# Performance work log

Measured on AMD Instinct MI355X. Metric: run time of the kernel, lower is better.

Reference implementation:

```python
import jax, jax.numpy as jnp
import numpy as np

N_NODES = 50000
N_EDGES = 800000
D_IN = 128
D_HID = 128
D_OUT = 128


def setup_inputs() -> dict:
    key = jax.random.key(0)
    ks = jax.random.split(key, 5)
    x = jax.random.normal(ks[0], (N_NODES, D_IN), dtype=jnp.float32)
    edge_index = jax.random.randint(ks[1], (2, N_EDGES), 0, N_NODES, dtype=jnp.int64)
    # Glorot-ish init for the two GCN linear weights (PyG uses glorot)
    W1 = jax.random.normal(ks[2], (D_IN, D_HID), dtype=jnp.float32) * (1.0 / np.sqrt(D_IN))
    b1 = jnp.zeros((D_HID,), dtype=jnp.float32)
    W2 = jax.random.normal(ks[3], (D_HID, D_OUT), dtype=jnp.float32) * (1.0 / np.sqrt(D_HID))
    b2 = jnp.zeros((D_OUT,), dtype=jnp.float32)
    return {"x": x, "edge_index": edge_index, "W1": W1, "b1": b1, "W2": W2, "b2": b2}


def _gcn_layer(x, W, b, src, dst, dinv):
    """PyG GCNConv: h = xW; out[j] = sum_{(i->j)} dinv[i]*dinv[j]*h[i] + dinv[j]^2*h[j] (self-loop) + b."""
    n = x.shape[0]
    h = x @ W                                   # [N, D_out]
    coef = (dinv[src] * dinv[dst])[:, None]     # [E, 1] symmetric norm
    msg = h[src] * coef                         # [E, D_out] gather + scale
    agg = jax.ops.segment_sum(msg, dst, num_segments=n)  # scatter-add
    agg = agg + h * (dinv * dinv)[:, None]      # self-loop contribution
    return agg + b


def reference(x, edge_index, W1, b1, W2, b2):
    src = edge_index[0]
    dst = edge_index[1]
    n = x.shape[0]
    # degree over target nodes, including the added self-loop (+1)
    deg = jax.ops.segment_sum(jnp.ones_like(dst, dtype=x.dtype), dst, num_segments=n) + 1.0
    dinv = jax.lax.rsqrt(deg)
    h = jax.nn.relu(_gcn_layer(x, W1, b1, src, dst, dinv))
    return _gcn_layer(h, W2, b2, src, dst, dinv)
```

## Files before the change

kernel.cpp:

```cpp
#include <hip/hip_runtime.h>
#include <hip/hip_fp16.h>

#define NN 50000
#define NE 800000
#define D 128
#define NBLK ((NN + 255) / 256)
#define NBLK_GEMM ((NN + 63) / 64)

typedef __attribute__((ext_vector_type(8))) _Float16 f16x8;
typedef __attribute__((ext_vector_type(8))) short short8;
typedef __attribute__((ext_vector_type(4))) float f32x4;

__global__ __launch_bounds__(256) void k_init(int* __restrict__ cnt,
                                              const float* __restrict__ W1, const float* __restrict__ W2,
                                              char* __restrict__ img1, char* __restrict__ img2) {
    int b = blockIdx.x;
    if (b < NBLK) {
        int i = b * 256 + threadIdx.x;
        if (i < NN) cnt[i] = 0;
    } else {
        int pb = b - NBLK;
        const float* W = (pb < 64) ? W1 : W2;
        char* img = (pb < 64) ? img1 : img2;
        int e = (pb & 63) * 256 + threadIdx.x;
        int k = e >> 7, n = e & 127;
        float f = W[e];
        __half hi = __float2half_rn(f);
        float rem = f - __half2float(hi);
        __half lo = __float2half_rn(rem);
        unsigned off = (unsigned)((n << 8) + (k << 1)) ^ (unsigned)((n & 7) << 4);
        *(__half*)(img + off) = hi;
        *(__half*)(img + 32768 + off) = lo;
    }
}

__global__ __launch_bounds__(256) void k_count(const int* __restrict__ dst, int* __restrict__ cnt,
                                               unsigned short* __restrict__ rank) {
    int e = blockIdx.x * 256 + threadIdx.x;
    if (e < NE) rank[e] = (unsigned short)atomicAdd(&cnt[dst[e]], 1);
}

__global__ __launch_bounds__(256) void k_scan_partial(const int* __restrict__ cnt, int* __restrict__ blockSums) {
    __shared__ int s[256];
    int t = threadIdx.x;
    int i = blockIdx.x * 256 + t;
    s[t] = (i < NN) ? cnt[i] : 0;
    __syncthreads();
    for (int off = 128; off > 0; off >>= 1) {
        if (t < off) s[t] += s[t + off];
        __syncthreads();
    }
    if (t == 0) blockSums[blockIdx.x] = s[0];
}

__global__ __launch_bounds__(256) void k_scan_final(const int* __restrict__ cnt, const int* __restrict__ blockSums,
                                                    int* __restrict__ row_ptr, float* __restrict__ dinv) {
    __shared__ int s[256];
    int t = threadIdx.x;

    s[t] = (t < NBLK && t < (int)blockIdx.x) ? blockSums[t] : 0;
    __syncthreads();
    for (int off = 128; off > 0; off >>= 1) {
        if (t < off) s[t] += s[t + off];
        __syncthreads();
    }
    int blockOff = s[0];
    __syncthreads();

    int i = blockIdx.x * 256 + t;
    int v = (i < NN) ? cnt[i] : 0;
    s[t] = v;
    __syncthreads();
    for (int off = 1; off < 256; off <<= 1) {
        int y = (t >= off) ? s[t - off] : 0;
        __syncthreads();
        s[t] += y;
        __syncthreads();
    }
    if (i < NN) {
        row_ptr[i] = s[t] - v + blockOff;
        dinv[i] = rsqrtf((float)v + 1.0f);
    }
    if (blockIdx.x == 0 && t == 0) row_ptr[NN] = NE;
}

template <bool RELU_IN, bool A_FP16>
static __device__ __forceinline__ void gemm_core(char* lds, const void* __restrict__ Av,
                                                 const char* __restrict__ wimg, __half* __restrict__ H,
                                                 int bid, int t) {
    {
        const float4* gv = (const float4*)wimg;
        float4* lv = (float4*)lds;
#pragma unroll
        for (int i = 0; i < 16; ++i) lv[i * 256 + t] = gv[i * 256 + t];
    }
    __syncthreads();

    const int lane = t & 63;
    const int wv = t >> 6;
    const int r0 = bid * 64 + wv * 16;
    const int rl = lane & 15;
    const int g = lane >> 4;
    int arow = r0 + rl;
    if (arow >= NN) arow = NN - 1;

    f32x4 acc[8];
#pragma unroll
    for (int j = 0; j < 8; ++j) acc[j] = (f32x4){0.f, 0.f, 0.f, 0.f};

#pragma unroll
    for (int ks = 0; ks < 4; ++ks) {
        f16x8 a;
        if (A_FP16) {
            const __half* A = (const __half*)Av;
            float4 raw = *(const float4*)(A + (size_t)arow * D + ks * 32 + g * 8);
            if (RELU_IN) {
                short8 s = __builtin_bit_cast(short8, raw);
#pragma unroll
                for (int i = 0; i < 8; ++i) s[i] = (s[i] & (short)0x8000) ? (short)0 : s[i];
                a = __builtin_bit_cast(f16x8, s);
            } else {
                a = __builtin_bit_cast(f16x8, raw);
            }
        } else {
            const float* A = (const float*)Av;
            const float* ar = A + (size_t)arow * D + ks * 32 + g * 8;
            float4 p0 = *(const float4*)ar;
            float4 p1 = *(const float4*)(ar + 4);
            float av8[8] = {p0.x, p0.y, p0.z, p0.w, p1.x, p1.y, p1.z, p1.w};
#pragma unroll
            for (int i = 0; i < 8; ++i) {
                float f = RELU_IN ? fmaxf(av8[i], 0.f) : av8[i];
                a[i] = (_Float16)f;
            }
        }
        const int kofs = (ks * 32 + g * 8) << 1;
#pragma unroll
        for (int j = 0; j < 8; ++j) {
            int n = j * 16 + rl;
            unsigned off = (unsigned)((n << 8) + kofs) ^ (unsigned)((n & 7) << 4);
            f16x8 bh = *(const f16x8*)(lds + off);
            f16x8 bl = *(const f16x8*)(lds + 32768 + off);
            acc[j] = __builtin_amdgcn_mfma_f32_16x16x32_f16(a, bh, acc[j], 0, 0, 0);
            acc[j] = __builtin_amdgcn_mfma_f32_16x16x32_f16(a, bl, acc[j], 0, 0, 0);
        }
    }

#pragma unroll
    for (int j = 0; j < 8; ++j) {
#pragma unroll
        for (int i = 0; i < 4; ++i) {
            int row = r0 + g * 4 + i;
            if (row < NN) H[(size_t)row * D + j * 16 + rl] = __float2half(acc[j][i]);
        }
    }
}

__global__ __launch_bounds__(256) void k_fill_gemm1(const int* __restrict__ src, const int* __restrict__ dst,
                                                    const unsigned short* __restrict__ rank,
                                                    const int* __restrict__ row_ptr,
                                                    unsigned short* __restrict__ csr,
                                                    const float* __restrict__ x, const char* __restrict__ wimg,
                                                    __half* __restrict__ H) {
    __shared__ char lds[65536];
    int bid = blockIdx.x;
    if (bid < NBLK_GEMM) {
        gemm_core<false, false>(lds, x, wimg, H, bid, threadIdx.x);
    } else {
        int e = (bid - NBLK_GEMM) * 256 + threadIdx.x;
        if (e < NE) {
            int d = dst[e];
            csr[row_ptr[d] + rank[e]] = (unsigned short)src[e];
        }
    }
}

template <bool RELU_IN, bool A_FP16>
__global__ __launch_bounds__(256) void k_mgemm(const void* __restrict__ Av, const char* __restrict__ wimg,
                                               __half* __restrict__ H) {
    __shared__ char lds[65536];
    gemm_core<RELU_IN, A_FP16>(lds, Av, wimg, H, blockIdx.x, threadIdx.x);
}

template <bool OUT_FP16>
__global__ __launch_bounds__(256) void k_pull(const __half* __restrict__ H, const float* __restrict__ dinv,
                                              const float* __restrict__ b, const int* __restrict__ row_ptr,
                                              const unsigned short* __restrict__ csr, void* __restrict__ outv) {
    int wid = (blockIdx.x * 256 + threadIdx.x) >> 6;
    int lane = threadIdx.x & 63;
    int node = __builtin_amdgcn_readfirstlane(wid);
    int rl = lane & 15;
    int g = lane >> 4;

    float dd = dinv[node];

    float2 a0 = {0.f, 0.f}, a1 = {0.f, 0.f}, a2 = {0.f, 0.f}, a3 = {0.f, 0.f};
    float2 c0b = {0.f, 0.f}, c1b = {0.f, 0.f}, c2b = {0.f, 0.f}, c3b = {0.f, 0.f};

    int beg = row_ptr[node];
    int end = row_ptr[node + 1];
    for (int i = beg + g; i < end; i += 8) {
        int i1 = i + 4;
        bool ok = i1 < end;
        int s0 = csr[i];
        int s1 = csr[ok ? i1 : i];
        float c0 = dinv[s0] * dd;
        float c1 = ok ? dinv[s1] * dd : 0.f;
        float4 raw0 = *(const float4*)(H + (size_t)s0 * D + rl * 8);
        float4 raw1 = *(const float4*)(H + (size_t)s1 * D + rl * 8);
        const __half2* h0 = (const __half2*)&raw0;
        const __half2* h1 = (const __half2*)&raw1;
        float2 f0 = __half22float2(h0[0]);
        float2 f1 = __half22float2(h0[1]);
        float2 f2 = __half22float2(h0[2]);
        float2 f3 = __half22float2(h0[3]);
        a0.x = fmaf(f0.x, c0, a0.x); a0.y = fmaf(f0.y, c0, a0.y);
        a1.x = fmaf(f1.x, c0, a1.x); a1.y = fmaf(f1.y, c0, a1.y);
        a2.x = fmaf(f2.x, c0, a2.x); a2.y = fmaf(f2.y, c0, a2.y);
        a3.x = fmaf(f3.x, c0, a3.x); a3.y = fmaf(f3.y, c0, a3.y);
        float2 g0 = __half22float2(h1[0]);
        float2 g1 = __half22float2(h1[1]);
        float2 g2 = __half22float2(h1[2]);
        float2 g3 = __half22float2(h1[3]);
        c0b.x = fmaf(g0.x, c1, c0b.x); c0b.y = fmaf(g0.y, c1, c0b.y);
        c1b.x = fmaf(g1.x, c1, c1b.x); c1b.y = fmaf(g1.y, c1, c1b.y);
        c2b.x = fmaf(g2.x, c1, c2b.x); c2b.y = fmaf(g2.y, c1, c2b.y);
        c3b.x = fmaf(g3.x, c1, c3b.x); c3b.y = fmaf(g3.y, c1, c3b.y);
    }
    a0.x += c0b.x; a0.y += c0b.y;
    a1.x += c1b.x; a1.y += c1b.y;
    a2.x += c2b.x; a2.y += c2b.y;
    a3.x += c3b.x; a3.y += c3b.y;

    float v[8] = {a0.x, a0.y, a1.x, a1.y, a2.x, a2.y, a3.x, a3.y};
#pragma unroll
    for (int i = 0; i < 8; ++i) {
        v[i] += __shfl_xor(v[i], 16);
        v[i] += __shfl_xor(v[i], 32);
    }

    if (g == 0) {
        float s2 = dd * dd;
        float4 raw = *(const float4*)(H + (size_t)node * D + rl * 8);
        const __half2* hh = (const __half2*)&raw;
        float2 s0 = __half22float2(hh[0]);
        float2 s1 = __half22float2(hh[1]);
        float2 s2v = __half22float2(hh[2]);
        float2 s3 = __half22float2(hh[3]);
        float4 b0 = ((const float4*)b)[rl * 2];
        float4 b1v = ((const float4*)b)[rl * 2 + 1];
        float r[8];
        r[0] = fmaf(s0.x, s2, v[0] + b0.x);
        r[1] = fmaf(s0.y, s2, v[1] + b0.y);
        r[2] = fmaf(s1.x, s2, v[2] + b0.z);
        r[3] = fmaf(s1.y, s2, v[3] + b0.w);
        r[4] = fmaf(s2v.x, s2, v[4] + b1v.x);
        r[5] = fmaf(s2v.y, s2, v[5] + b1v.y);
        r[6] = fmaf(s3.x, s2, v[6] + b1v.z);
        r[7] = fmaf(s3.y, s2, v[7] + b1v.w);
        if (OUT_FP16) {
            __half* out = (__half*)outv;
            __half2 o[4];
            o[0] = __floats2half2_rn(r[0], r[1]);
            o[1] = __floats2half2_rn(r[2], r[3]);
            o[2] = __floats2half2_rn(r[4], r[5]);
            o[3] = __floats2half2_rn(r[6], r[7]);
            *(float4*)(out + (size_t)node * D + rl * 8) = *(float4*)o;
        } else {
            float* out = (float*)outv;
            float* op = out + (size_t)node * D + rl * 8;
            *(float4*)op = make_float4(r[0], r[1], r[2], r[3]);
            *(float4*)(op + 4) = make_float4(r[4], r[5], r[6], r[7]);
        }
    }
}

extern "C" void kernel_launch(void* const* d_in, const int* in_sizes, int n_in,
                              void* d_out, int out_size, void* d_ws, size_t ws_size,
                              hipStream_t stream) {
    const float* x  = (const float*)d_in[0];
    const int*   ei = (const int*)d_in[1];
    const float* W1 = (const float*)d_in[2];
    const float* b1 = (const float*)d_in[3];
    const float* W2 = (const float*)d_in[4];
    const float* b2 = (const float*)d_in[5];
    float* out = (float*)d_out;

    const int* src = ei;
    const int* dst = ei + NE;

    char* ws = (char*)d_ws;
    int*    cnt       = (int*)   (ws + 0);
    int*    row_ptr   = (int*)   (ws + 204800);
    int*    blockSums = (int*)   (ws + 409600);
    float*  dinv      = (float*) (ws + 410624);
    char*   wimg1     = (char*)  (ws + 614400);
    char*   wimg2     = (char*)  (ws + 679936);
    unsigned short* rank = (unsigned short*)(ws + 745472);
    unsigned short* csr  = (unsigned short*)(ws + 2345472);
    __half* h         = (__half*)(ws + 3945472);
    __half* h2        = (__half*)(ws + 16745472);

    const int nBlkEdge = (NE + 255) / 256;
    const int nBlkPull = NN / 4;

    k_init<<<NBLK + 128, 256, 0, stream>>>(cnt, W1, W2, wimg1, wimg2);
    k_count<<<nBlkEdge, 256, 0, stream>>>(dst, cnt, rank);
    k_scan_partial<<<NBLK, 256, 0, stream>>>(cnt, blockSums);
    k_scan_final<<<NBLK, 256, 0, stream>>>(cnt, blockSums, row_ptr, dinv);
    k_fill_gemm1<<<NBLK_GEMM + nBlkEdge, 256, 0, stream>>>(src, dst, rank, row_ptr, csr, x, wimg1, h);
    k_pull<true><<<nBlkPull, 256, 0, stream>>>(h, dinv, b1, row_ptr, csr, h2);
    k_mgemm<true, true><<<NBLK_GEMM, 256, 0, stream>>>(h2, wimg2, h);
    k_pull<false><<<nBlkPull, 256, 0, stream>>>(h, dinv, b2, row_ptr, csr, out);
}
```

Before: 227.5 us.

## Drop split-fp16 weight low part and use nontemporal loads/stores

Stops keeping a residual low half of each weight in fp16, which halves the LDS weight image and the MFMA count in both GEMMs and shrinks shared memory to 32KB per block. It also switches activation loads in the GEMM, and output stores in both the GEMM and the pull kernel, to nontemporal variants to reduce cache pollution. The cost is lower weight precision, since the weights are now rounded to fp16 only, and this can increase error against the fp32 reference. The nontemporal H stores may also hurt the later pull kernels, which read H back.

```diff
diff --git a/kernel.cpp b/kernel.cpp
--- a/kernel.cpp
+++ b/kernel.cpp
@@ -24,13 +24,9 @@
         char* img = (pb < 64) ? img1 : img2;
         int e = (pb & 63) * 256 + threadIdx.x;
         int k = e >> 7, n = e & 127;
-        float f = W[e];
-        __half hi = __float2half_rn(f);
-        float rem = f - __half2float(hi);
-        __half lo = __float2half_rn(rem);
+        __half hi = __float2half_rn(W[e]);
         unsigned off = (unsigned)((n << 8) + (k << 1)) ^ (unsigned)((n & 7) << 4);
         *(__half*)(img + off) = hi;
-        *(__half*)(img + 32768 + off) = lo;
     }
 }
 
@@ -92,7 +88,7 @@
         const float4* gv = (const float4*)wimg;
         float4* lv = (float4*)lds;
 #pragma unroll
-        for (int i = 0; i < 16; ++i) lv[i * 256 + t] = gv[i * 256 + t];
+        for (int i = 0; i < 8; ++i) lv[i * 256 + t] = gv[i * 256 + t];
     }
     __syncthreads();
 
@@ -113,7 +109,7 @@
         f16x8 a;
         if (A_FP16) {
             const __half* A = (const __half*)Av;
-            float4 raw = *(const float4*)(A + (size_t)arow * D + ks * 32 + g * 8);
+            f32x4 raw = __builtin_nontemporal_load((const f32x4*)(A + (size_t)arow * D + ks * 32 + g * 8));
             if (RELU_IN) {
                 short8 s = __builtin_bit_cast(short8, raw);
 #pragma unroll
@@ -125,8 +121,8 @@
         } else {
             const float* A = (const float*)Av;
             const float* ar = A + (size_t)arow * D + ks * 32 + g * 8;
-            float4 p0 = *(const float4*)ar;
-            float4 p1 = *(const float4*)(ar + 4);
+            f32x4 p0 = __builtin_nontemporal_load((const f32x4*)ar);
+            f32x4 p1 = __builtin_nontemporal_load((const f32x4*)(ar + 4));
             float av8[8] = {p0.x, p0.y, p0.z, p0.w, p1.x, p1.y, p1.z, p1.w};
 #pragma unroll
             for (int i = 0; i < 8; ++i) {
@@ -140,9 +136,7 @@
             int n = j * 16 + rl;
             unsigned off = (unsigned)((n << 8) + kofs) ^ (unsigned)((n & 7) << 4);
             f16x8 bh = *(const f16x8*)(lds + off);
-            f16x8 bl = *(const f16x8*)(lds + 32768 + off);
             acc[j] = __builtin_amdgcn_mfma_f32_16x16x32_f16(a, bh, acc[j], 0, 0, 0);
-            acc[j] = __builtin_amdgcn_mfma_f32_16x16x32_f16(a, bl, acc[j], 0, 0, 0);
         }
     }
 
@@ -151,7 +145,10 @@
 #pragma unroll
         for (int i = 0; i < 4; ++i) {
             int row = r0 + g * 4 + i;
-            if (row < NN) H[(size_t)row * D + j * 16 + rl] = __float2half(acc[j][i]);
+            if (row < NN) {
+                unsigned short bits = __half_as_ushort(__float2half(acc[j][i]));
+                __builtin_nontemporal_store(bits, (unsigned short*)(H + (size_t)row * D + j * 16 + rl));
+            }
         }
     }
 }
@@ -162,7 +159,7 @@
                                                     unsigned short* __restrict__ csr,
                                                     const float* __restrict__ x, const char* __restrict__ wimg,
                                                     __half* __restrict__ H) {
-    __shared__ char lds[65536];
+    __shared__ char lds[32768];
     int bid = blockIdx.x;
     if (bid < NBLK_GEMM) {
         gemm_core<false, false>(lds, x, wimg, H, bid, threadIdx.x);
@@ -178,7 +175,7 @@
 template <bool RELU_IN, bool A_FP16>
 __global__ __launch_bounds__(256) void k_mgemm(const void* __restrict__ Av, const char* __restrict__ wimg,
                                                __half* __restrict__ H) {
-    __shared__ char lds[65536];
+    __shared__ char lds[32768];
     gemm_core<RELU_IN, A_FP16>(lds, Av, wimg, H, blockIdx.x, threadIdx.x);
 }
 
@@ -260,17 +257,20 @@
         r[7] = fmaf(s3.y, s2, v[7] + b1v.w);
         if (OUT_FP16) {
             __half* out = (__half*)outv;
-            __half2 o[4];
-            o[0] = __floats2half2_rn(r[0], r[1]);
-            o[1] = __floats2half2_rn(r[2], r[3]);
-            o[2] = __floats2half2_rn(r[4], r[5]);
-            o[3] = __floats2half2_rn(r[6], r[7]);
-            *(float4*)(out + (size_t)node * D + rl * 8) = *(float4*)o;
+            __half2 o0 = __floats2half2_rn(r[0], r[1]);
+            __half2 o1 = __floats2half2_rn(r[2], r[3]);
+            __half2 o2 = __floats2half2_rn(r[4], r[5]);
+            __half2 o3 = __floats2half2_rn(r[6], r[7]);
+            f32x4 ov = {__builtin_bit_cast(float, o0), __builtin_bit_cast(float, o1),
+                        __builtin_bit_cast(float, o2), __builtin_bit_cast(float, o3)};
+            __builtin_nontemporal_store(ov, (f32x4*)(out + (size_t)node * D + rl * 8));
         } else {
             float* out = (float*)outv;
             float* op = out + (size_t)node * D + rl * 8;
-            *(float4*)op = make_float4(r[0], r[1], r[2], r[3]);
-            *(float4*)(op + 4) = make_float4(r[4], r[5], r[6], r[7]);
+            f32x4 r0v = {r[0], r[1], r[2], r[3]};
+            f32x4 r1v = {r[4], r[5], r[6], r[7]};
+            __builtin_nontemporal_store(r0v, (f32x4*)op);
+            __builtin_nontemporal_store(r1v, (f32x4*)(op + 4));
         }
     }
 }
@@ -295,11 +295,11 @@
     int*    blockSums = (int*)   (ws + 409600);
     float*  dinv      = (float*) (ws + 410624);
     char*   wimg1     = (char*)  (ws + 614400);
-    char*   wimg2     = (char*)  (ws + 679936);
-    unsigned short* rank = (unsigned short*)(ws + 745472);
-    unsigned short* csr  = (unsigned short*)(ws + 2345472);
-    __half* h         = (__half*)(ws + 3945472);
-    __half* h2        = (__half*)(ws + 16745472);
+    char*   wimg2     = (char*)  (ws + 647168);
+    unsigned short* rank = (unsigned short*)(ws + 679936);
+    unsigned short* csr  = (unsigned short*)(ws + 2279936);
+    __half* h         = (__half*)(ws + 3879936);
+    __half* h2        = (__half*)(ws + 16679936);
 
     const int nBlkEdge = (NE + 255) / 256;
     const int nBlkPull = NN / 4;
```

Result: faster. 222.6 us (-2.1%).
